# Kernel optimization log

Measured on AMD Instinct MI355X. Metric: run time of the kernel, lower is better.

## Reference

```python
import jax, jax.numpy as jnp
import numpy as np

N = 20000      # nodes
E = 320000     # directed edges (before self-loops)
IN, HID, HEADS, OUT = 512, 256, 4, 256
NEG_SLOPE = 0.2  # PyG GATConv default


def setup_inputs() -> dict:
    key = jax.random.key(0)
    ks = jax.random.split(key, 10)
    x = jax.random.normal(ks[0], (N, IN), jnp.float32)
    edge_index = jax.random.randint(ks[1], (2, E), 0, N, jnp.int32)
    W1 = jax.random.normal(ks[2], (IN, HEADS * HID), jnp.float32) / np.sqrt(IN).astype(np.float32)
    att_src1 = jax.random.normal(ks[3], (HEADS, HID), jnp.float32) * 0.1
    att_dst1 = jax.random.normal(ks[4], (HEADS, HID), jnp.float32) * 0.1
    b1 = jnp.zeros((HEADS * HID,), jnp.float32)
    W2 = jax.random.normal(ks[5], (HEADS * HID, OUT), jnp.float32) / np.sqrt(HEADS * HID).astype(np.float32)
    att_src2 = jax.random.normal(ks[6], (1, OUT), jnp.float32) * 0.1
    att_dst2 = jax.random.normal(ks[7], (1, OUT), jnp.float32) * 0.1
    b2 = jnp.zeros((OUT,), jnp.float32)
    return {"x": x, "edge_index": edge_index, "W1": W1, "att_src1": att_src1,
            "att_dst1": att_dst1, "b1": b1, "W2": W2, "att_src2": att_src2,
            "att_dst2": att_dst2, "b2": b2}


def _segment_softmax(logits, seg, num_segments):
    # softmax over edges grouped by destination node (per head)
    m = jax.ops.segment_max(logits, seg, num_segments=num_segments)
    ex = jnp.exp(logits - m[seg])
    s = jax.ops.segment_sum(ex, seg, num_segments=num_segments)
    return ex / (s[seg] + 1e-16)


def _gat_conv(x, src, dst, W, att_src, att_dst, bias, heads, ch, num_nodes, concat):
    # PyG GATConv: h = W x (per head); alpha_e = softmax_dst(LeakyReLU(a_s.h_src + a_d.h_dst))
    h = (x @ W).reshape(num_nodes, heads, ch)          # [N,H,C]
    a_s = (h * att_src).sum(-1)                        # [N,H]
    a_d = (h * att_dst).sum(-1)                        # [N,H]
    logits = jax.nn.leaky_relu(a_s[src] + a_d[dst], NEG_SLOPE)   # [E,H]
    alpha = _segment_softmax(logits, dst, num_nodes)             # [E,H]
    msg = h[src] * alpha[:, :, None]                             # [E,H,C]
    out = jax.ops.segment_sum(msg, dst, num_segments=num_nodes)  # [N,H,C]
    out = out.reshape(num_nodes, heads * ch) if concat else out.mean(axis=1)
    return out + bias


def reference(x, edge_index, W1, att_src1, att_dst1, b1, W2, att_src2, att_dst2, b2):
    # add self-loops (PyG default add_self_loops=True)
    loop = jnp.arange(N, dtype=edge_index.dtype)
    src = jnp.concatenate([edge_index[0], loop])
    dst = jnp.concatenate([edge_index[1], loop])
    h = jax.nn.elu(_gat_conv(x, src, dst, W1, att_src1, att_dst1, b1, HEADS, HID, N, True))
    return _gat_conv(h, src, dst, W2, att_src2, att_dst2, b2, 1, OUT, N, False)
```

## Files before the change

### kernel.cpp

```cpp
#include <hip/hip_runtime.h>
#include <hip/hip_bf16.h>
#include <cfloat>
#include <math.h>

#define N_NODES 20000
#define M_PAD   20096
#define N_EDGES 320000
#define TOT_E   (N_EDGES + N_NODES)
#define IN_F    512
#define HID     256
#define HEADS   4
#define OUT_F   256
#define H1DIM   (HEADS * HID)
#define NEG_SLOPE 0.2f

typedef __attribute__((ext_vector_type(8))) __bf16 bf16x8;
typedef __attribute__((ext_vector_type(4))) __bf16 bf16x4;
typedef __attribute__((ext_vector_type(4))) float f32x4;

__device__ __forceinline__ float lrelu(float x) { return x >= 0.f ? x : NEG_SLOPE * x; }

__global__ void k_count(const int* __restrict__ ei, int* __restrict__ deg) {
  int e = blockIdx.x * 256 + threadIdx.x;
  if (e >= TOT_E) return;
  int dst = (e < N_EDGES) ? ei[N_EDGES + e] : (e - N_EDGES);
  atomicAdd(&deg[dst], 1);
}

__global__ void k_scan(const int* __restrict__ deg, int* __restrict__ off) {
  __shared__ int part[256];
  int tid = threadIdx.x;
  const int chunk = (N_NODES + 255) / 256;
  int s0 = tid * chunk;
  int s1 = s0 + chunk; if (s1 > N_NODES) s1 = N_NODES; if (s0 > N_NODES) s0 = N_NODES;
  int s = 0;
  for (int i = s0; i < s1; ++i) s += deg[i];
  part[tid] = s;
  __syncthreads();
  for (int d = 1; d < 256; d <<= 1) {
    int v = (tid >= d) ? part[tid - d] : 0;
    __syncthreads();
    part[tid] += v;
    __syncthreads();
  }
  int run = (tid == 0) ? 0 : part[tid - 1];
  for (int i = s0; i < s1; ++i) { off[i] = run; run += deg[i]; }
  if (tid == 255) off[N_NODES] = run;
}

__global__ void k_fill(const int* __restrict__ ei, const int* __restrict__ off,
                       int* __restrict__ cur, int* __restrict__ csr_src) {
  int e = blockIdx.x * 256 + threadIdx.x;
  if (e >= TOT_E) return;
  int src, dst;
  if (e < N_EDGES) { src = ei[e]; dst = ei[N_EDGES + e]; }
  else             { src = dst = e - N_EDGES; }
  int pos = atomicAdd(&cur[dst], 1);
  csr_src[off[dst] + pos] = src;
}

__global__ void k_f2b(const float* __restrict__ in, __bf16* __restrict__ out, int n4) {
  int i = blockIdx.x * 256 + threadIdx.x;
  if (i >= n4) return;
  float4 v = ((const float4*)in)[i];
  bf16x4 o = { (__bf16)v.x, (__bf16)v.y, (__bf16)v.z, (__bf16)v.w };
  ((bf16x4*)out)[i] = o;
}

__global__ void k_tr_f2b(const float* __restrict__ in, __bf16* __restrict__ out,
                         int R, int Cc) {
  __shared__ float tile[32][33];
  int c0 = blockIdx.x * 32, r0 = blockIdx.y * 32;
  int tx = threadIdx.x & 31, ty = threadIdx.x >> 5;
  for (int rr = ty; rr < 32; rr += 8)
    tile[rr][tx] = in[(size_t)(r0 + rr) * Cc + c0 + tx];
  __syncthreads();
  for (int rr = ty; rr < 32; rr += 8)
    out[(size_t)(c0 + rr) * R + r0 + tx] = (__bf16)tile[tx][rr];
}

__global__ __launch_bounds__(256) void k_gemm_bf16(
    const __bf16* __restrict__ A,
    const __bf16* __restrict__ Bt,
    __bf16* __restrict__ Cb,
    int M, int N, int K)
{
  __shared__ char lds[32768];
  char* As = lds;
  char* Bs = lds + 16384;

  const int t = threadIdx.x;
  const int lane = t & 63;
  const int wid = t >> 6;
  const int wm = wid >> 1, wn = wid & 1;
  const int row0 = blockIdx.y * 128;
  const int col0 = blockIdx.x * 128;

  f32x4 acc[4][4];
#pragma unroll
  for (int i = 0; i < 4; ++i)
#pragma unroll
    for (int j = 0; j < 4; ++j) acc[i][j] = (f32x4){0.f, 0.f, 0.f, 0.f};

  for (int k0 = 0; k0 < K; k0 += 64) {
#pragma unroll
    for (int i = 0; i < 4; ++i) {
      int j = i * 256 + t;
      int r = j >> 3;
      int cc = (j & 7) ^ (r & 7);
      const __bf16* gp = A + (size_t)(row0 + r) * K + k0 + cc * 8;
      __builtin_amdgcn_global_load_lds(
          (const __attribute__((address_space(1))) void*)gp,
          (__attribute__((address_space(3))) void*)(As + j * 16), 16, 0, 0);
    }
#pragma unroll
    for (int i = 0; i < 4; ++i) {
      int j = i * 256 + t;
      int r = j >> 3;
      int cc = (j & 7) ^ (r & 7);
      const __bf16* gp = Bt + (size_t)(col0 + r) * K + k0 + cc * 8;
      __builtin_amdgcn_global_load_lds(
          (const __attribute__((address_space(1))) void*)gp,
          (__attribute__((address_space(3))) void*)(Bs + j * 16), 16, 0, 0);
    }
    __syncthreads();

#pragma unroll
    for (int ks = 0; ks < 2; ++ks) {
      bf16x8 af[4], bfr[4];
#pragma unroll
      for (int i = 0; i < 4; ++i) {
        int rA = wm * 64 + i * 16 + (lane & 15);
        int chA = (ks * 4 + (lane >> 4)) ^ (rA & 7);
        af[i] = *(const bf16x8*)(As + rA * 128 + chA * 16);
        int rB = wn * 64 + i * 16 + (lane & 15);
        int chB = (ks * 4 + (lane >> 4)) ^ (rB & 7);
        bfr[i] = *(const bf16x8*)(Bs + rB * 128 + chB * 16);
      }
#pragma unroll
      for (int i = 0; i < 4; ++i)
#pragma unroll
        for (int jn = 0; jn < 4; ++jn)
          acc[i][jn] = __builtin_amdgcn_mfma_f32_16x16x32_bf16(
              af[i], bfr[jn], acc[i][jn], 0, 0, 0);
    }
    __syncthreads();
  }

#pragma unroll
  for (int i = 0; i < 4; ++i) {
    int growb = row0 + wm * 64 + i * 16 + (lane >> 4) * 4;
#pragma unroll
    for (int jn = 0; jn < 4; ++jn) {
      int gcol = col0 + wn * 64 + jn * 16 + (lane & 15);
#pragma unroll
      for (int r = 0; r < 4; ++r) {
        int grow = growb + r;
        if (grow < M) Cb[(size_t)grow * N + gcol] = (__bf16)acc[i][jn][r];
      }
    }
  }
}

__global__ void k_attn1(const __bf16* __restrict__ h1b, const float* __restrict__ att_s,
                        const float* __restrict__ att_d, float* __restrict__ as,
                        float* __restrict__ ad) {
  int n = blockIdx.x;
  int t = threadIdx.x;
  int head = t >> 6, lane = t & 63;
  bf16x4 hv = *(const bf16x4*)(h1b + (size_t)n * H1DIM + t * 4);
  float4 sv = *(const float4*)(att_s + t * 4);
  float4 dv = *(const float4*)(att_d + t * 4);
  float h0 = (float)hv[0], h1 = (float)hv[1], h2 = (float)hv[2], h3 = (float)hv[3];
  float ss = h0 * sv.x + h1 * sv.y + h2 * sv.z + h3 * sv.w;
  float sd = h0 * dv.x + h1 * dv.y + h2 * dv.z + h3 * dv.w;
#pragma unroll
  for (int d = 32; d; d >>= 1) { ss += __shfl_xor(ss, d); sd += __shfl_xor(sd, d); }
  if (lane == 0) { as[n * HEADS + head] = ss; ad[n * HEADS + head] = sd; }
}

__global__ void k_attn2(const __bf16* __restrict__ h2b, const float* __restrict__ att_s,
                        const float* __restrict__ att_d, float* __restrict__ as,
                        float* __restrict__ ad) {
  int n = blockIdx.x;
  int lane = threadIdx.x;
  bf16x4 hv = *(const bf16x4*)(h2b + (size_t)n * OUT_F + lane * 4);
  float4 sv = *(const float4*)(att_s + lane * 4);
  float4 dv = *(const float4*)(att_d + lane * 4);
  float h0 = (float)hv[0], h1 = (float)hv[1], h2 = (float)hv[2], h3 = (float)hv[3];
  float ss = h0 * sv.x + h1 * sv.y + h2 * sv.z + h3 * sv.w;
  float sd = h0 * dv.x + h1 * dv.y + h2 * dv.z + h3 * dv.w;
#pragma unroll
  for (int d = 32; d; d >>= 1) { ss += __shfl_xor(ss, d); sd += __shfl_xor(sd, d); }
  if (lane == 0) { as[n] = ss; ad[n] = sd; }
}

__global__ __launch_bounds__(128) void k_agg1(
    const int* __restrict__ off, const int* __restrict__ csr_src,
    const __bf16* __restrict__ h1b, const float* __restrict__ as,
    const float* __restrict__ ad, const float* __restrict__ b1,
    __bf16* __restrict__ heluB) {
  int n = blockIdx.x;
  int t = threadIdx.x;
  int wave = t >> 6, lane = t & 63;
  int beg = off[n], end = off[n + 1];
  float4 advv = *(const float4*)&ad[n * 4];
  float adv[4] = {advv.x, advv.y, advv.z, advv.w};

  __shared__ float wl[64][4];
  __shared__ int sl[64];
  __shared__ float ssumW[2][4];

  const int head = t >> 5;
  const int myh = t & 3;
  const int idx = t >> 2;

  float acc[8] = {0.f, 0.f, 0.f, 0.f, 0.f, 0.f, 0.f, 0.f};
  float psum = 0.f;

  for (int e0 = beg; e0 < end; e0 += 64) {
    int cnt = min(64, end - e0);
    if (idx < cnt) {
      int s = csr_src[e0 + idx];
      float w = __expf(lrelu(as[s * 4 + myh] + adv[myh]));
      wl[idx][myh] = w;
      psum += w;
      if (myh == 0) sl[idx] = s;
    }
    if (idx + 32 < cnt) {
      int s = csr_src[e0 + idx + 32];
      float w = __expf(lrelu(as[s * 4 + myh] + adv[myh]));
      wl[idx + 32][myh] = w;
      psum += w;
      if (myh == 0) sl[idx + 32] = s;
    }
    __syncthreads();
#pragma unroll 4
    for (int e = 0; e < cnt; ++e) {
      float wv = wl[e][head];
      int s = sl[e];
      bf16x8 hv = *(const bf16x8*)(h1b + (size_t)s * H1DIM + t * 8);
#pragma unroll
      for (int k = 0; k < 8; ++k) acc[k] += wv * (float)hv[k];
    }
    __syncthreads();
  }

#pragma unroll
  for (int d = 4; d <= 32; d <<= 1) psum += __shfl_xor(psum, d);
  if (lane < 4) ssumW[wave][lane] = psum;
  __syncthreads();
  float sume = ssumW[0][head] + ssumW[1][head];
  float inv = 1.f / (sume + 1e-16f);

  float4 bv0 = *(const float4*)(b1 + t * 8);
  float4 bv1 = *(const float4*)(b1 + t * 8 + 4);
  float bb[8] = {bv0.x, bv0.y, bv0.z, bv0.w, bv1.x, bv1.y, bv1.z, bv1.w};
  bf16x8 o;
#pragma unroll
  for (int k = 0; k < 8; ++k) {
    float v = acc[k] * inv + bb[k];
    v = v > 0.f ? v : expm1f(v);
    o[k] = (__bf16)v;
  }
  *(bf16x8*)(heluB + (size_t)n * H1DIM + t * 8) = o;
}

__global__ void k_agg2(const int* __restrict__ off, const int* __restrict__ csr_src,
                       const __bf16* __restrict__ h2b, const float* __restrict__ as,
                       const float* __restrict__ ad, const float* __restrict__ b2,
                       float* __restrict__ out) {
  int n = blockIdx.x;
  int lane = threadIdx.x;
  int beg = off[n], end = off[n + 1];
  float adv = ad[n];

  __shared__ float wl[64];
  __shared__ int sl[64];
  float acc[4] = {0.f, 0.f, 0.f, 0.f};
  float psum = 0.f;
  for (int e0 = beg; e0 < end; e0 += 64) {
    int cnt = min(64, end - e0);
    if (lane < cnt) {
      int s = csr_src[e0 + lane];
      float w = __expf(lrelu(as[s] + adv));
      wl[lane] = w;
      sl[lane] = s;
      psum += w;
    }
    __syncthreads();
#pragma unroll 4
    for (int e = 0; e < cnt; ++e) {
      float wv = wl[e];
      int s = sl[e];
      bf16x4 hv = *(const bf16x4*)(h2b + (size_t)s * OUT_F + lane * 4);
      acc[0] += wv * (float)hv[0];
      acc[1] += wv * (float)hv[1];
      acc[2] += wv * (float)hv[2];
      acc[3] += wv * (float)hv[3];
    }
    __syncthreads();
  }
#pragma unroll
  for (int d = 32; d; d >>= 1) psum += __shfl_xor(psum, d);
  float inv = 1.f / (psum + 1e-16f);
  float4 bv = *(const float4*)(b2 + lane * 4);
  float4 o = { acc[0] * inv + bv.x, acc[1] * inv + bv.y,
               acc[2] * inv + bv.z, acc[3] * inv + bv.w };
  *(float4*)(out + (size_t)n * OUT_F + lane * 4) = o;
}

extern "C" void kernel_launch(void* const* d_in, const int* in_sizes, int n_in,
                              void* d_out, int out_size, void* d_ws, size_t ws_size,
                              hipStream_t stream) {
  const float* x      = (const float*)d_in[0];
  const int*   ei     = (const int*)d_in[1];
  const float* W1     = (const float*)d_in[2];
  const float* att_s1 = (const float*)d_in[3];
  const float* att_d1 = (const float*)d_in[4];
  const float* b1     = (const float*)d_in[5];
  const float* W2     = (const float*)d_in[6];
  const float* att_s2 = (const float*)d_in[7];
  const float* att_d2 = (const float*)d_in[8];
  const float* b2     = (const float*)d_in[9];
  float* out = (float*)d_out;

  char* w = (char*)d_ws;
  auto alloc = [&](size_t bytes) {
    char* p = w;
    w += (bytes + 255) & ~(size_t)255;
    return p;
  };
  int*    deg   = (int*)alloc((size_t)N_NODES * 4);
  int*    off   = (int*)alloc((size_t)(N_NODES + 1) * 4);
  int*    cur   = (int*)alloc((size_t)N_NODES * 4);
  int*    csr   = (int*)alloc((size_t)TOT_E * 4);
  float*  as1   = (float*)alloc((size_t)N_NODES * HEADS * 4);
  float*  ad1   = (float*)alloc((size_t)N_NODES * HEADS * 4);
  float*  as2   = (float*)alloc((size_t)N_NODES * 4);
  float*  ad2   = (float*)alloc((size_t)N_NODES * 4);
  __bf16* xb    = (__bf16*)alloc((size_t)M_PAD * IN_F * 2);
  __bf16* w1t   = (__bf16*)alloc((size_t)H1DIM * IN_F * 2);
  __bf16* w2t   = (__bf16*)alloc((size_t)OUT_F * H1DIM * 2);
  __bf16* h1b   = (__bf16*)alloc((size_t)M_PAD * H1DIM * 2);
  __bf16* heluB = (__bf16*)alloc((size_t)M_PAD * H1DIM * 2);
  __bf16* h2b   = (__bf16*)alloc((size_t)M_PAD * OUT_F * 2);
  if ((size_t)(w - (char*)d_ws) > ws_size) return;

  hipMemsetAsync(deg, 0, (size_t)N_NODES * 4, stream);
  hipMemsetAsync(cur, 0, (size_t)N_NODES * 4, stream);

  k_count<<<(TOT_E + 255) / 256, 256, 0, stream>>>(ei, deg);
  k_scan<<<1, 256, 0, stream>>>(deg, off);
  k_fill<<<(TOT_E + 255) / 256, 256, 0, stream>>>(ei, off, cur, csr);

  int n4 = N_NODES * IN_F / 4;
  k_f2b<<<(n4 + 255) / 256, 256, 0, stream>>>(x, xb, n4);
  k_tr_f2b<<<dim3(H1DIM / 32, IN_F / 32), 256, 0, stream>>>(W1, w1t, IN_F, H1DIM);
  k_tr_f2b<<<dim3(OUT_F / 32, H1DIM / 32), 256, 0, stream>>>(W2, w2t, H1DIM, OUT_F);

  k_gemm_bf16<<<dim3(H1DIM / 128, M_PAD / 128), 256, 0, stream>>>(
      xb, w1t, h1b, N_NODES, H1DIM, IN_F);
  k_attn1<<<N_NODES, 256, 0, stream>>>(h1b, att_s1, att_d1, as1, ad1);
  k_agg1<<<N_NODES, 128, 0, stream>>>(off, csr, h1b, as1, ad1, b1, heluB);

  k_gemm_bf16<<<dim3(OUT_F / 128, M_PAD / 128), 256, 0, stream>>>(
      heluB, w2t, h2b, N_NODES, OUT_F, H1DIM);
  k_attn2<<<N_NODES, 64, 0, stream>>>(h2b, att_s2, att_d2, as2, ad2);
  k_agg2<<<N_NODES, 64, 0, stream>>>(off, csr, h2b, as2, ad2, b2, out);
}
```

Baseline: 297.3 us.

## Split GAT aggregation into edge-weight pass and column-sliced gather kernels

Each aggregation kernel is replaced by two kernels. The first computes per-edge exp-logits and per-node inverse sums into workspace buffers. The second gathers neighbor features with one wave per node per column slice, processing several edges concurrently across lane subgroups and reducing them with shuffles. This removes shared-memory staging and block syncs and raises memory-level parallelism for low-degree nodes, at the cost of an extra launch and extra global traffic for the weight arrays.

```diff
diff --git a/kernel.cpp b/kernel.cpp
--- a/kernel.cpp
+++ b/kernel.cpp
@@ -195,119 +195,146 @@
   if (lane == 0) { as[n] = ss; ad[n] = sd; }
 }
 
-__global__ __launch_bounds__(128) void k_agg1(
-    const int* __restrict__ off, const int* __restrict__ csr_src,
-    const __bf16* __restrict__ h1b, const float* __restrict__ as,
-    const float* __restrict__ ad, const float* __restrict__ b1,
-    __bf16* __restrict__ heluB) {
+__global__ void k_w1(const int* __restrict__ off, const int* __restrict__ csr,
+                     const float* __restrict__ as, const float* __restrict__ ad,
+                     float* __restrict__ wn, float* __restrict__ inv) {
   int n = blockIdx.x;
-  int t = threadIdx.x;
-  int wave = t >> 6, lane = t & 63;
+  int lane = threadIdx.x;
   int beg = off[n], end = off[n + 1];
-  float4 advv = *(const float4*)&ad[n * 4];
-  float adv[4] = {advv.x, advv.y, advv.z, advv.w};
-
-  __shared__ float wl[64][4];
-  __shared__ int sl[64];
-  __shared__ float ssumW[2][4];
-
-  const int head = t >> 5;
-  const int myh = t & 3;
-  const int idx = t >> 2;
-
-  float acc[8] = {0.f, 0.f, 0.f, 0.f, 0.f, 0.f, 0.f, 0.f};
-  float psum = 0.f;
-
-  for (int e0 = beg; e0 < end; e0 += 64) {
-    int cnt = min(64, end - e0);
-    if (idx < cnt) {
-      int s = csr_src[e0 + idx];
-      float w = __expf(lrelu(as[s * 4 + myh] + adv[myh]));
-      wl[idx][myh] = w;
-      psum += w;
-      if (myh == 0) sl[idx] = s;
-    }
-    if (idx + 32 < cnt) {
-      int s = csr_src[e0 + idx + 32];
-      float w = __expf(lrelu(as[s * 4 + myh] + adv[myh]));
-      wl[idx + 32][myh] = w;
-      psum += w;
-      if (myh == 0) sl[idx + 32] = s;
-    }
-    __syncthreads();
-#pragma unroll 4
-    for (int e = 0; e < cnt; ++e) {
-      float wv = wl[e][head];
-      int s = sl[e];
-      bf16x8 hv = *(const bf16x8*)(h1b + (size_t)s * H1DIM + t * 8);
-#pragma unroll
-      for (int k = 0; k < 8; ++k) acc[k] += wv * (float)hv[k];
-    }
-    __syncthreads();
-  }
-
-#pragma unroll
-  for (int d = 4; d <= 32; d <<= 1) psum += __shfl_xor(psum, d);
-  if (lane < 4) ssumW[wave][lane] = psum;
-  __syncthreads();
-  float sume = ssumW[0][head] + ssumW[1][head];
-  float inv = 1.f / (sume + 1e-16f);
-
-  float4 bv0 = *(const float4*)(b1 + t * 8);
-  float4 bv1 = *(const float4*)(b1 + t * 8 + 4);
-  float bb[8] = {bv0.x, bv0.y, bv0.z, bv0.w, bv1.x, bv1.y, bv1.z, bv1.w};
-  bf16x8 o;
-#pragma unroll
-  for (int k = 0; k < 8; ++k) {
-    float v = acc[k] * inv + bb[k];
-    v = v > 0.f ? v : expm1f(v);
-    o[k] = (__bf16)v;
-  }
-  *(bf16x8*)(heluB + (size_t)n * H1DIM + t * 8) = o;
-}
-
-__global__ void k_agg2(const int* __restrict__ off, const int* __restrict__ csr_src,
-                       const __bf16* __restrict__ h2b, const float* __restrict__ as,
-                       const float* __restrict__ ad, const float* __restrict__ b2,
-                       float* __restrict__ out) {
+  float4 adv = *(const float4*)&ad[n * 4];
+  float p0 = 0.f, p1 = 0.f, p2 = 0.f, p3 = 0.f;
+  for (int p = beg + lane; p < end; p += 64) {
+    int s = csr[p];
+    float4 av = *(const float4*)&as[s * 4];
+    float w0 = __expf(lrelu(av.x + adv.x));
+    float w1 = __expf(lrelu(av.y + adv.y));
+    float w2 = __expf(lrelu(av.z + adv.z));
+    float w3 = __expf(lrelu(av.w + adv.w));
+    p0 += w0; p1 += w1; p2 += w2; p3 += w3;
+    float4 wv = {w0, w1, w2, w3};
+    *(float4*)&wn[(size_t)p * 4] = wv;
+  }
+#pragma unroll
+  for (int d = 32; d; d >>= 1) {
+    p0 += __shfl_xor(p0, d); p1 += __shfl_xor(p1, d);
+    p2 += __shfl_xor(p2, d); p3 += __shfl_xor(p3, d);
+  }
+  if (lane == 0) {
+    float4 iv = {1.f / (p0 + 1e-16f), 1.f / (p1 + 1e-16f),
+                 1.f / (p2 + 1e-16f), 1.f / (p3 + 1e-16f)};
+    *(float4*)&inv[n * 4] = iv;
+  }
+}
+
+__global__ void k_w2(const int* __restrict__ off, const int* __restrict__ csr,
+                     const float* __restrict__ as, const float* __restrict__ ad,
+                     float* __restrict__ wn, float* __restrict__ inv) {
   int n = blockIdx.x;
   int lane = threadIdx.x;
   int beg = off[n], end = off[n + 1];
   float adv = ad[n];
-
-  __shared__ float wl[64];
-  __shared__ int sl[64];
-  float acc[4] = {0.f, 0.f, 0.f, 0.f};
-  float psum = 0.f;
-  for (int e0 = beg; e0 < end; e0 += 64) {
-    int cnt = min(64, end - e0);
-    if (lane < cnt) {
-      int s = csr_src[e0 + lane];
-      float w = __expf(lrelu(as[s] + adv));
-      wl[lane] = w;
-      sl[lane] = s;
-      psum += w;
+  float ps = 0.f;
+  for (int p = beg + lane; p < end; p += 64) {
+    int s = csr[p];
+    float w = __expf(lrelu(as[s] + adv));
+    wn[p] = w;
+    ps += w;
+  }
+#pragma unroll
+  for (int d = 32; d; d >>= 1) ps += __shfl_xor(ps, d);
+  if (lane == 0) inv[n] = 1.f / (ps + 1e-16f);
+}
+
+__global__ __launch_bounds__(256) void k_gather1(
+    const int* __restrict__ off, const int* __restrict__ csr,
+    const __bf16* __restrict__ h1b, const float* __restrict__ wn,
+    const float* __restrict__ inv, const float* __restrict__ b1,
+    __bf16* __restrict__ heluB) {
+  int bid = blockIdx.x;
+  int slice = bid & 7;
+  int grp = bid >> 3;
+  int wid = threadIdx.x >> 6, lane = threadIdx.x & 63;
+  int n = grp * 4 + wid;
+  int cb = slice * 128;
+  int head = slice >> 1;
+  int sub = lane >> 4, cg = lane & 15;
+  int beg = off[n], end = off[n + 1];
+
+  float acc[8] = {0.f, 0.f, 0.f, 0.f, 0.f, 0.f, 0.f, 0.f};
+  const __bf16* hb = h1b + cb + cg * 8;
+#pragma unroll 2
+  for (int p = beg; p < end; p += 4) {
+    int e = p + sub;
+    float w = 0.f; int s = 0;
+    if (e < end) { s = csr[e]; w = wn[(size_t)e * 4 + head]; }
+    bf16x8 hv = *(const bf16x8*)(hb + (size_t)s * H1DIM);
+#pragma unroll
+    for (int k = 0; k < 8; ++k) acc[k] += w * (float)hv[k];
+  }
+#pragma unroll
+  for (int k = 0; k < 8; ++k) {
+    acc[k] += __shfl_xor(acc[k], 16);
+    acc[k] += __shfl_xor(acc[k], 32);
+  }
+  if (sub == 0) {
+    float iv = inv[n * 4 + head];
+    float4 b0 = *(const float4*)(b1 + cb + cg * 8);
+    float4 b1v = *(const float4*)(b1 + cb + cg * 8 + 4);
+    float bb[8] = {b0.x, b0.y, b0.z, b0.w, b1v.x, b1v.y, b1v.z, b1v.w};
+    bf16x8 o;
+#pragma unroll
+    for (int k = 0; k < 8; ++k) {
+      float v = acc[k] * iv + bb[k];
+      v = v > 0.f ? v : expm1f(v);
+      o[k] = (__bf16)v;
     }
-    __syncthreads();
-#pragma unroll 4
-    for (int e = 0; e < cnt; ++e) {
-      float wv = wl[e];
-      int s = sl[e];
-      bf16x4 hv = *(const bf16x4*)(h2b + (size_t)s * OUT_F + lane * 4);
-      acc[0] += wv * (float)hv[0];
-      acc[1] += wv * (float)hv[1];
-      acc[2] += wv * (float)hv[2];
-      acc[3] += wv * (float)hv[3];
-    }
-    __syncthreads();
-  }
-#pragma unroll
-  for (int d = 32; d; d >>= 1) psum += __shfl_xor(psum, d);
-  float inv = 1.f / (psum + 1e-16f);
-  float4 bv = *(const float4*)(b2 + lane * 4);
-  float4 o = { acc[0] * inv + bv.x, acc[1] * inv + bv.y,
-               acc[2] * inv + bv.z, acc[3] * inv + bv.w };
-  *(float4*)(out + (size_t)n * OUT_F + lane * 4) = o;
+    *(bf16x8*)(heluB + (size_t)n * H1DIM + cb + cg * 8) = o;
+  }
+}
+
+__global__ __launch_bounds__(256) void k_gather2(
+    const int* __restrict__ off, const int* __restrict__ csr,
+    const __bf16* __restrict__ h2b, const float* __restrict__ wn,
+    const float* __restrict__ inv, const float* __restrict__ b2,
+    float* __restrict__ out) {
+  int bid = blockIdx.x;
+  int slice = bid & 3;
+  int grp = bid >> 2;
+  int wid = threadIdx.x >> 6, lane = threadIdx.x & 63;
+  int n = grp * 4 + wid;
+  int cb = slice * 64;
+  int sub = lane >> 3, cg = lane & 7;
+  int beg = off[n], end = off[n + 1];
+
+  float acc[8] = {0.f, 0.f, 0.f, 0.f, 0.f, 0.f, 0.f, 0.f};
+  const __bf16* hb = h2b + cb + cg * 8;
+#pragma unroll 2
+  for (int p = beg; p < end; p += 8) {
+    int e = p + sub;
+    float w = 0.f; int s = 0;
+    if (e < end) { s = csr[e]; w = wn[e]; }
+    bf16x8 hv = *(const bf16x8*)(hb + (size_t)s * OUT_F);
+#pragma unroll
+    for (int k = 0; k < 8; ++k) acc[k] += w * (float)hv[k];
+  }
+#pragma unroll
+  for (int k = 0; k < 8; ++k) {
+    acc[k] += __shfl_xor(acc[k], 8);
+    acc[k] += __shfl_xor(acc[k], 16);
+    acc[k] += __shfl_xor(acc[k], 32);
+  }
+  if (sub == 0) {
+    float iv = inv[n];
+    float4 b0 = *(const float4*)(b2 + cb + cg * 8);
+    float4 b1v = *(const float4*)(b2 + cb + cg * 8 + 4);
+    float* op = out + (size_t)n * OUT_F + cb + cg * 8;
+    float4 o0 = {acc[0] * iv + b0.x, acc[1] * iv + b0.y,
+                 acc[2] * iv + b0.z, acc[3] * iv + b0.w};
+    float4 o1 = {acc[4] * iv + b1v.x, acc[5] * iv + b1v.y,
+                 acc[6] * iv + b1v.z, acc[7] * iv + b1v.w};
+    *(float4*)op = o0;
+    *(float4*)(op + 4) = o1;
+  }
 }
 
 extern "C" void kernel_launch(void* const* d_in, const int* in_sizes, int n_in,
@@ -339,6 +366,10 @@
   float*  ad1   = (float*)alloc((size_t)N_NODES * HEADS * 4);
   float*  as2   = (float*)alloc((size_t)N_NODES * 4);
   float*  ad2   = (float*)alloc((size_t)N_NODES * 4);
+  float*  wn1   = (float*)alloc((size_t)TOT_E * HEADS * 4);
+  float*  inv1  = (float*)alloc((size_t)N_NODES * HEADS * 4);
+  float*  wn2   = (float*)alloc((size_t)TOT_E * 4);
+  float*  inv2  = (float*)alloc((size_t)N_NODES * 4);
   __bf16* xb    = (__bf16*)alloc((size_t)M_PAD * IN_F * 2);
   __bf16* w1t   = (__bf16*)alloc((size_t)H1DIM * IN_F * 2);
   __bf16* w2t   = (__bf16*)alloc((size_t)OUT_F * H1DIM * 2);
@@ -362,10 +393,12 @@
   k_gemm_bf16<<<dim3(H1DIM / 128, M_PAD / 128), 256, 0, stream>>>(
       xb, w1t, h1b, N_NODES, H1DIM, IN_F);
   k_attn1<<<N_NODES, 256, 0, stream>>>(h1b, att_s1, att_d1, as1, ad1);
-  k_agg1<<<N_NODES, 128, 0, stream>>>(off, csr, h1b, as1, ad1, b1, heluB);
+  k_w1<<<N_NODES, 64, 0, stream>>>(off, csr, as1, ad1, wn1, inv1);
+  k_gather1<<<(N_NODES / 4) * 8, 256, 0, stream>>>(off, csr, h1b, wn1, inv1, b1, heluB);
 
   k_gemm_bf16<<<dim3(OUT_F / 128, M_PAD / 128), 256, 0, stream>>>(
       heluB, w2t, h2b, N_NODES, OUT_F, H1DIM);
   k_attn2<<<N_NODES, 64, 0, stream>>>(h2b, att_s2, att_d2, as2, ad2);
-  k_agg2<<<N_NODES, 64, 0, stream>>>(off, csr, h2b, as2, ad2, b2, out);
-}
+  k_w2<<<N_NODES, 64, 0, stream>>>(off, csr, as2, ad2, wn2, inv2);
+  k_gather2<<<(N_NODES / 4) * 4, 256, 0, stream>>>(off, csr, h2b, wn2, inv2, b2, out);
+}
```

Result: slower. 324.0 us (+9.0%).
